# Kernel tuning notes

Hardware: AMD Instinct MI355X
Metric: run time of the kernel (lower is better)

## Reference

```python
import jax, jax.numpy as jnp
import numpy as np

B, N, C_FEAT = 2, 1024, 64
S, K, K_FP = 512, 32, 3
D_MODEL, N_HEAD = 128, 4
EPS_BN = 1e-5


def square_distance(src, dst):
    # src [B,N,3], dst [B,M,3] -> [B,N,M], same expansion as torch version
    d = -2.0 * jnp.einsum('bnc,bmc->bnm', src, dst)
    d = d + jnp.sum(src ** 2, -1)[:, :, None]
    d = d + jnp.sum(dst ** 2, -1)[:, None, :]
    return d


def gather_points(points, idx):
    # points [B,N,C], idx [B,...] int -> [B,...,C]  (index_points)
    return jax.vmap(lambda p, i: p[i])(points, idx)


def fps(xyz, n_samples):
    # furthest point sampling, deterministic start at index 0
    Bs, Np, _ = xyz.shape
    def step(carry, _):
        dist, far = carry
        centroid = jax.vmap(lambda p, i: p[i])(xyz, far)  # [B,3]
        d = jnp.sum((xyz - centroid[:, None, :]) ** 2, -1)
        dist = jnp.minimum(dist, d)
        new_far = jnp.argmax(dist, -1).astype(jnp.int32)
        return (dist, new_far), far
    init = (jnp.full((Bs, Np), 1e10, xyz.dtype), jnp.zeros((Bs,), jnp.int32))
    _, idxs = jax.lax.scan(step, init, None, length=n_samples)
    return idxs.T  # [B,S]


def knn(nsample, xyz, new_xyz):
    d = square_distance(new_xyz, xyz)
    _, idx = jax.lax.top_k(-d, nsample)
    return idx  # [B, n_query, nsample]


def setup_inputs() -> dict:
    key = jax.random.key(0)
    ks = jax.random.split(key, 12)
    Din = 2 * C_FEAT + 3  # 131 = 3 + 2*channels (PreExtraction in_channels)
    def lin(k, fan_in, shape):
        return (jax.random.normal(k, shape, jnp.float32) / np.sqrt(fan_in)).astype(jnp.float32)
    z = lambda n: jnp.zeros((n,), jnp.float32)
    return {
        'xyz': jax.random.normal(ks[0], (B, N, 3), jnp.float32),
        'feats': jax.random.normal(ks[1], (B, N, C_FEAT), jnp.float32),
        'affine_alpha': jnp.ones((1, 1, 1, C_FEAT + 3), jnp.float32),
        'affine_beta': jnp.zeros((1, 1, 1, C_FEAT + 3), jnp.float32),
        'W_t': lin(ks[2], Din, (Din, D_MODEL)), 'b_t': z(D_MODEL),
        'bn_g': jnp.ones((D_MODEL,), jnp.float32), 'bn_b': z(D_MODEL),
        'Wq': lin(ks[3], D_MODEL, (D_MODEL, D_MODEL)), 'bq': z(D_MODEL),
        'Wk': lin(ks[4], D_MODEL, (D_MODEL, D_MODEL)), 'bk': z(D_MODEL),
        'Wv': lin(ks[5], D_MODEL, (D_MODEL, D_MODEL)), 'bv': z(D_MODEL),
        'Wo': lin(ks[6], D_MODEL, (D_MODEL, D_MODEL)), 'bo': z(D_MODEL),
        'Wp1': lin(ks[7], 3, (3, D_MODEL)), 'bp1': z(D_MODEL),
        'Wp2': lin(ks[8], D_MODEL, (D_MODEL, N_HEAD)), 'bp2': z(N_HEAD),
    }


def reference(xyz, feats, affine_alpha, affine_beta, W_t, b_t, bn_g, bn_b,
              Wq, bq, Wk, bk, Wv, bv, Wo, bo, Wp1, bp1, Wp2, bp2):
    # ---- LocalGrouper (FPS + KNN + gather + center-normalize + affine) ----
    fps_idx = fps(xyz, S)                       # [B,S]
    new_xyz = gather_points(xyz, fps_idx)       # [B,S,3]
    anchor_feats = gather_points(feats, fps_idx)  # [B,S,C]
    idx = knn(K, xyz, new_xyz)                  # [B,S,K]
    grouped_xyz = gather_points(xyz, idx)       # [B,S,K,3]
    grouped_pts = gather_points(feats, idx)     # [B,S,K,C]
    grouped = jnp.concatenate([grouped_pts, grouped_xyz], -1)  # [B,S,K,C+3]
    mean = jnp.mean(grouped, axis=2, keepdims=True)
    std = jnp.std((grouped - mean).reshape(B, -1), axis=-1, ddof=1)[:, None, None, None]
    grouped = (grouped - mean) / (std + 1e-5)
    grouped = affine_alpha * grouped + affine_beta
    anchor_rep = jnp.broadcast_to(anchor_feats[:, :, None, :], (B, S, K, C_FEAT))
    new_points = jnp.concatenate([grouped, anchor_rep], -1)  # [B,S,K,2C+3]
    # ---- PreExtraction transfer (1x1 conv + BN(eval) + ReLU) + max over K ----
    y = jnp.einsum('bskd,do->bsko', new_points, W_t) + b_t
    y = y * (bn_g / jnp.sqrt(1.0 + EPS_BN)) + bn_b  # BN with running stats (0,1)
    y = jax.nn.relu(y)
    v_k = jnp.max(y, axis=2)                    # [B,S,D_MODEL]
    # ---- PointNetFeaturePropagation (KNN-3 inverse-distance interp) ----
    idx_fp = knn(K_FP, new_xyz, xyz)            # [B,N,3]
    sqrd = square_distance(xyz, new_xyz)        # [B,N,S]
    d_near = jnp.clip(jnp.take_along_axis(sqrd, idx_fp, axis=2), 1e-10, None)
    w = 1.0 / d_near
    w = w / jnp.sum(w, -1, keepdims=True)
    grouped_v = gather_points(v_k, idx_fp)      # [B,N,3,D]
    v_q = jnp.einsum('bnk,bnkc->bnc', w, grouped_v)  # [B,N,D]
    # ---- PointTransformerCrossAttention ----
    Dh = D_MODEL // N_HEAD
    qh = (v_q @ Wq + bq).reshape(B, N, N_HEAD, Dh)
    kh = (v_k @ Wk + bk).reshape(B, S, N_HEAD, Dh)
    vh = (v_k @ Wv + bv).reshape(B, S, N_HEAD, Dh)
    rel = xyz[:, :, None, :] - new_xyz[:, None, :, :]         # [B,N,S,3]
    rpe = jax.nn.relu(rel @ Wp1 + bp1) @ Wp2 + bp2            # [B,N,S,H]
    energy = jnp.einsum('bihd,bjhd->bhij', qh, kh) / jnp.sqrt(jnp.float32(Dh))
    attn = jax.nn.softmax(energy + rpe.transpose(0, 3, 1, 2), axis=-1)
    out = jnp.einsum('bhij,bjhd->bihd', attn, vh).reshape(B, N, D_MODEL)
    return out @ Wo + bo
```

## Files before the change

### kernel.cpp

```cpp
#include <hip/hip_runtime.h>
#include <math.h>

namespace {

constexpr int B  = 2;
constexpr int N  = 1024;
constexpr int CF = 64;
constexpr int S  = 512;
constexpr int K  = 32;
constexpr int DM = 128;
constexpr int NH = 4;
constexpr int DH = 32;
constexpr int GC = 67;
constexpr int DIN = 131;
constexpr int DPAD = 132;
constexpr int EPAD = 516;

typedef float f2 __attribute__((ext_vector_type(2)));

__device__ inline float max3f(float a, float b, float c) { return fmaxf(fmaxf(a, b), c); }
__device__ inline unsigned min3u(unsigned a, unsigned b, unsigned c) { return min(min(a, b), c); }

template <int CTRL>
__device__ inline float dpp_mov_f(float v) {
  return __int_as_float(__builtin_amdgcn_update_dpp(0, __float_as_int(v), CTRL, 0xF, 0xF, true));
}
template <int CTRL>
__device__ inline unsigned dpp_mov_self_u(unsigned v) {
  return (unsigned)__builtin_amdgcn_update_dpp((int)v, (int)v, CTRL, 0xF, 0xF, false);
}

__global__ void __launch_bounds__(64, 1)
fps_kernel(const float* __restrict__ xyz, int* __restrict__ fps_idx,
           float* __restrict__ new_xyz) {
  const int b = blockIdx.x;
  const int lane = threadIdx.x;
  __shared__ __align__(16) float4 pts4[N];
  __shared__ int farhist[S];
  for (int p = lane; p < N; p += 64) {
    pts4[p] = make_float4(xyz[b*N*3 + p*3+0], xyz[b*N*3 + p*3+1], xyz[b*N*3 + p*3+2], 0.0f);
  }
  __syncthreads();
  f2 X[8], Y[8], Z[8];
  float dist[16];
  #pragma unroll
  for (int j = 0; j < 8; ++j) {
    const float4 a = pts4[(2*j)*64 + lane];
    const float4 c = pts4[(2*j+1)*64 + lane];
    X[j] = f2{a.x, c.x}; Y[j] = f2{a.y, c.y}; Z[j] = f2{a.z, c.z};
  }
  #pragma unroll
  for (int k = 0; k < 16; ++k) dist[k] = 1e10f;
  int far = 0;
  for (int s = 0; s < S; ++s) {
    if (lane == 0) farhist[s] = far;
    const float4 c = pts4[far];
    const f2 cx = f2{c.x, c.x}, cy = f2{c.y, c.y}, cz = f2{c.z, c.z};
    #pragma unroll
    for (int j = 0; j < 8; ++j) {
      const f2 dx = X[j] - cx, dy = Y[j] - cy, dz = Z[j] - cz;
      const f2 q = dx*dx + dy*dy + dz*dz;
      dist[2*j]   = fminf(dist[2*j],   q.x);
      dist[2*j+1] = fminf(dist[2*j+1], q.y);
    }
    const float l0 = max3f(dist[0],  dist[1],  dist[2]);
    const float l1 = max3f(dist[3],  dist[4],  dist[5]);
    const float l2 = max3f(dist[6],  dist[7],  dist[8]);
    const float l3 = max3f(dist[9],  dist[10], dist[11]);
    const float l4 = max3f(dist[12], dist[13], dist[14]);
    float mv = fmaxf(max3f(l0, l1, l2), max3f(l3, l4, dist[15]));
    mv = fmaxf(mv, dpp_mov_f<0x111>(mv));
    mv = fmaxf(mv, dpp_mov_f<0x112>(mv));
    mv = fmaxf(mv, dpp_mov_f<0x114>(mv));
    mv = fmaxf(mv, dpp_mov_f<0x118>(mv));
    mv = fmaxf(mv, dpp_mov_f<0x142>(mv));
    mv = fmaxf(mv, dpp_mov_f<0x143>(mv));
    const float maxv = __int_as_float(__builtin_amdgcn_readlane(__float_as_int(mv), 63));
    unsigned cnd[16];
    #pragma unroll
    for (int k = 0; k < 16; ++k) {
      cnd[k] = (dist[k] == maxv) ? (unsigned)(k*64 + lane) : 0xFFFFFFFFu;
    }
    const unsigned u0 = min3u(cnd[0],  cnd[1],  cnd[2]);
    const unsigned u1 = min3u(cnd[3],  cnd[4],  cnd[5]);
    const unsigned u2 = min3u(cnd[6],  cnd[7],  cnd[8]);
    const unsigned u3 = min3u(cnd[9],  cnd[10], cnd[11]);
    const unsigned u4 = min3u(cnd[12], cnd[13], cnd[14]);
    unsigned cand = min(min3u(u0, u1, u2), min3u(u3, u4, cnd[15]));
    cand = min(cand, dpp_mov_self_u<0x111>(cand));
    cand = min(cand, dpp_mov_self_u<0x112>(cand));
    cand = min(cand, dpp_mov_self_u<0x114>(cand));
    cand = min(cand, dpp_mov_self_u<0x118>(cand));
    cand = min(cand, dpp_mov_self_u<0x142>(cand));
    cand = min(cand, dpp_mov_self_u<0x143>(cand));
    far = __builtin_amdgcn_readlane((int)cand, 63);
  }
  __syncthreads();
  for (int s = lane; s < S; s += 64) {
    const int f = farhist[s];
    const float4 c = pts4[f];
    fps_idx[b*S+s] = f;
    new_xyz[(b*S+s)*3+0] = c.x;
    new_xyz[(b*S+s)*3+1] = c.y;
    new_xyz[(b*S+s)*3+2] = c.z;
  }
}

__global__ void knn_kernel(const float* __restrict__ xyz, const float* __restrict__ new_xyz,
                           int* __restrict__ knn_idx) {
  const int b = blockIdx.y;
  const int tid = threadIdx.x;
  const int wave = tid >> 6, lane = tid & 63;
  const int s = blockIdx.x * 4 + wave;
  __shared__ float pts[N*3];
  for (int i = tid; i < N*3; i += 256) pts[i] = xyz[b*N*3 + i];
  __syncthreads();
  const float qx = new_xyz[(b*S+s)*3+0], qy = new_xyz[(b*S+s)*3+1], qz = new_xyz[(b*S+s)*3+2];
  const float qn = qx*qx + qy*qy + qz*qz;
  float d[16];
  #pragma unroll
  for (int j = 0; j < 16; ++j) {
    const int p = j*64 + lane;
    const float px = pts[p*3+0], py = pts[p*3+1], pz = pts[p*3+2];
    const float dot = qx*px + qy*py + qz*pz;
    const float pn  = px*px + py*py + pz*pz;
    d[j] = (-2.0f*dot + qn) + pn;
  }
  unsigned mask = 0xFFFFu;
  for (int k = 0; k < K; ++k) {
    float bv = INFINITY; int bj = 0;
    #pragma unroll
    for (int j = 0; j < 16; ++j) {
      if (((mask >> j) & 1u) && d[j] < bv) { bv = d[j]; bj = j; }
    }
    int bp = bj*64 + lane;
    #pragma unroll
    for (int m = 1; m < 64; m <<= 1) {
      const float ov = __shfl_xor(bv, m);
      const int   op = __shfl_xor(bp, m);
      if (ov < bv || (ov == bv && op < bp)) { bv = ov; bp = op; }
    }
    if (lane == 0) knn_idx[(b*S+s)*K + k] = bp;
    if ((bp & 63) == lane) mask &= ~(1u << (bp >> 6));
  }
}

__global__ void group_stats_kernel(const float* __restrict__ feats, const float* __restrict__ xyz,
                                   const int* __restrict__ knn_idx, float* __restrict__ mean_out,
                                   float2* __restrict__ partials) {
  const int bs = blockIdx.x;
  const int b = bs / S;
  const int t = threadIdx.x;
  __shared__ int sidx[K];
  if (t < K) sidx[t] = knn_idx[bs*K + t];
  __syncthreads();
  float v[K];
  float ls = 0.0f, lsq = 0.0f;
  if (t < GC) {
    float sum = 0.0f;
    #pragma unroll
    for (int k = 0; k < K; ++k) {
      const int p = sidx[k];
      const float g = (t < CF) ? feats[(b*N+p)*CF + t] : xyz[(b*N+p)*3 + (t-CF)];
      v[k] = g; sum += g;
    }
    const float mean = sum * (1.0f/K);
    mean_out[bs*GC + t] = mean;
    #pragma unroll
    for (int k = 0; k < K; ++k) {
      const float c = v[k] - mean;
      ls += c; lsq += c*c;
    }
  }
  __shared__ float r1[128], r2[128];
  r1[t] = ls; r2[t] = lsq;
  __syncthreads();
  for (int off = 64; off >= 1; off >>= 1) {
    if (t < off) { r1[t] += r1[t+off]; r2[t] += r2[t+off]; }
    __syncthreads();
  }
  if (t == 0) partials[bs] = make_float2(r1[0], r2[0]);
}

__global__ void stats_kernel(const float2* __restrict__ partials, float* __restrict__ invstd) {
  const int b = blockIdx.x;
  const int lane = threadIdx.x;
  double su = 0.0, sq = 0.0;
  for (int i = lane; i < S; i += 64) {
    const float2 p = partials[b*S+i];
    su += (double)p.x; sq += (double)p.y;
  }
  #pragma unroll
  for (int m = 1; m < 64; m <<= 1) { su += __shfl_xor(su, m); sq += __shfl_xor(sq, m); }
  if (lane == 0) {
    const double nn = (double)S * K * GC;
    const double var = (sq - su*su/nn) / (nn - 1.0);
    invstd[b] = 1.0f / ((float)sqrt(var) + 1e-5f);
  }
}

__global__ void transfer_kernel(const float* __restrict__ feats, const float* __restrict__ xyz,
                                const int* __restrict__ knn_idx, const int* __restrict__ fps_idx,
                                const float* __restrict__ mean_in, const float* __restrict__ invstd,
                                const float* __restrict__ alpha, const float* __restrict__ beta,
                                const float* __restrict__ W_t, const float* __restrict__ b_t,
                                const float* __restrict__ bn_g, const float* __restrict__ bn_b,
                                const float* __restrict__ Wk, const float* __restrict__ bk,
                                const float* __restrict__ Wv, const float* __restrict__ bv,
                                float* __restrict__ v_k, float* __restrict__ kpb,
                                float* __restrict__ vpb) {
  const int bs = blockIdx.x;
  const int b = bs / S;
  const int t = threadIdx.x;
  __shared__ __align__(16) float np_s[K][DPAD];
  __shared__ float vrow[DM];
  __shared__ int sidx[K];
  __shared__ int sanchor;
  if (t < K) sidx[t] = knn_idx[bs*K + t];
  if (t == 0) sanchor = fps_idx[bs];
  __syncthreads();
  const float sinv = invstd[b];
  for (int k = 0; k < K; ++k) {
    const int p = sidx[k];
    for (int c = t; c < DPAD; c += 128) {
      float val = 0.0f;
      if (c < GC) {
        const float g = (c < CF) ? feats[(b*N+p)*CF + c] : xyz[(b*N+p)*3 + (c-CF)];
        val = (g - mean_in[bs*GC + c]) * sinv * alpha[c] + beta[c];
      } else if (c < DIN) {
        val = feats[(b*N+sanchor)*CF + (c - GC)];
      }
      np_s[k][c] = val;
    }
  }
  __syncthreads();
  float acc[K];
  const float bt = b_t[t];
  #pragma unroll
  for (int k = 0; k < K; ++k) acc[k] = bt;
  for (int d4 = 0; d4 < DPAD/4; ++d4) {
    const int d = d4*4;
    const float w0 = W_t[(d+0)*DM + t];
    const float w1 = W_t[(d+1)*DM + t];
    const float w2 = W_t[(d+2)*DM + t];
    const float w3 = (d+3 < DIN) ? W_t[(d+3)*DM + t] : 0.0f;
    #pragma unroll
    for (int k = 0; k < K; ++k) {
      const float4 f = *reinterpret_cast<const float4*>(&np_s[k][d]);
      acc[k] = acc[k] + f.x*w0 + f.y*w1 + f.z*w2 + f.w*w3;
    }
  }
  const float scale = bn_g[t] / sqrtf(1.0f + 1e-5f);
  const float shift = bn_b[t];
  float mx = -INFINITY;
  #pragma unroll
  for (int k = 0; k < K; ++k) {
    const float y = fmaxf(acc[k]*scale + shift, 0.0f);
    mx = fmaxf(mx, y);
  }
  v_k[bs*DM + t] = mx;
  vrow[t] = mx;
  __syncthreads();
  float acck = bk[t], accv = bv[t];
  for (int d = 0; d < DM; ++d) {
    const float f = vrow[d];
    acck += f * Wk[d*DM + t];
    accv += f * Wv[d*DM + t];
  }
  kpb[bs*DM + t] = acck;
  vpb[bs*DM + t] = accv;
}

__global__ void interp_kernel(const float* __restrict__ xyz, const float* __restrict__ new_xyz,
                              const float* __restrict__ v_k, const float* __restrict__ Wq,
                              const float* __restrict__ bq, float* __restrict__ qbuf) {
  const int b = blockIdx.y;
  const int tid = threadIdx.x;
  const int wave = tid >> 6, lane = tid & 63;
  const int n = blockIdx.x*4 + wave;
  __shared__ float pts[S*3];
  __shared__ float vqs[4][DM];
  for (int i = tid; i < S*3; i += 256) pts[i] = xyz ? new_xyz[b*S*3 + i] : 0.0f;
  __syncthreads();
  const float qx = xyz[(b*N+n)*3+0], qy = xyz[(b*N+n)*3+1], qz = xyz[(b*N+n)*3+2];
  const float qn = qx*qx + qy*qy + qz*qz;
  float d[8];
  #pragma unroll
  for (int j = 0; j < 8; ++j) {
    const int p = j*64 + lane;
    const float px = pts[p*3+0], py = pts[p*3+1], pz = pts[p*3+2];
    const float dot = qx*px + qy*py + qz*pz;
    const float pn  = px*px + py*py + pz*pz;
    d[j] = (-2.0f*dot + qn) + pn;
  }
  unsigned mask = 0xFFu;
  float sd[3]; int sp[3];
  #pragma unroll
  for (int k = 0; k < 3; ++k) {
    float bv = INFINITY; int bj = 0;
    #pragma unroll
    for (int j = 0; j < 8; ++j) {
      if (((mask >> j) & 1u) && d[j] < bv) { bv = d[j]; bj = j; }
    }
    int bp = bj*64 + lane;
    #pragma unroll
    for (int m = 1; m < 64; m <<= 1) {
      const float ov = __shfl_xor(bv, m);
      const int   op = __shfl_xor(bp, m);
      if (ov < bv || (ov == bv && op < bp)) { bv = ov; bp = op; }
    }
    sd[k] = bv; sp[k] = bp;
    if ((bp & 63) == lane) mask &= ~(1u << (bp >> 6));
  }
  float w0 = 1.0f / fmaxf(sd[0], 1e-10f);
  float w1 = 1.0f / fmaxf(sd[1], 1e-10f);
  float w2 = 1.0f / fmaxf(sd[2], 1e-10f);
  const float wsum = w0 + w1 + w2;
  w0 /= wsum; w1 /= wsum; w2 /= wsum;
  const float* vk0 = v_k + (b*S + sp[0])*DM;
  const float* vk1 = v_k + (b*S + sp[1])*DM;
  const float* vk2 = v_k + (b*S + sp[2])*DM;
  #pragma unroll
  for (int c = lane; c < DM; c += 64) {
    vqs[wave][c] = w0*vk0[c] + w1*vk1[c] + w2*vk2[c];
  }
  __syncthreads();
  const float* row = vqs[wave];
  #pragma unroll
  for (int half = 0; half < 2; ++half) {
    const int c = lane + half*64;
    float acc = bq[c];
    for (int d = 0; d < DM; ++d) acc += row[d] * Wq[d*DM + c];
    qbuf[(b*N+n)*DM + c] = acc;
  }
}

__global__ void attn_kernel(const float* __restrict__ xyz, const float* __restrict__ new_xyz,
                            const float* __restrict__ qb, const float* __restrict__ kp,
                            const float* __restrict__ vp, const float* __restrict__ Wp1,
                            const float* __restrict__ bp1, const float* __restrict__ Wp2,
                            const float* __restrict__ bp2, const float* __restrict__ Wo,
                            const float* __restrict__ bo, float* __restrict__ out) {
  const int bn = blockIdx.x;
  const int b = bn / N;
  const int t = threadIdx.x;
  __shared__ __align__(16) float e[NH][EPAD];
  __shared__ float qn_s[DM];
  __shared__ float oa[DM];
  __shared__ float ssum[NH];
  qn_s[t] = qb[bn*DM + t];
  __syncthreads();
  const float qx = xyz[bn*3+0], qy = xyz[bn*3+1], qz = xyz[bn*3+2];
  const float rs = 0.17677669529663687f;
  for (int j = t; j < S; j += 128) {
    const float px = new_xyz[(b*S+j)*3+0], py = new_xyz[(b*S+j)*3+1], pz = new_xyz[(b*S+j)*3+2];
    const float rx = qx-px, ry = qy-py, rz = qz-pz;
    float r0 = bp2[0], r1 = bp2[1], r2 = bp2[2], r3 = bp2[3];
    for (int m = 0; m < DM; ++m) {
      float hm = rx*Wp1[m] + ry*Wp1[DM+m] + rz*Wp1[2*DM+m] + bp1[m];
      hm = fmaxf(hm, 0.0f);
      r0 += hm*Wp2[m*NH+0]; r1 += hm*Wp2[m*NH+1];
      r2 += hm*Wp2[m*NH+2]; r3 += hm*Wp2[m*NH+3];
    }
    const float rpe[NH] = {r0, r1, r2, r3};
    #pragma unroll
    for (int h = 0; h < NH; ++h) {
      const float* kr = kp + (b*S+j)*DM + h*DH;
      const float* qr = qn_s + h*DH;
      float acc = 0.0f;
      #pragma unroll
      for (int dd = 0; dd < DH; ++dd) acc += qr[dd]*kr[dd];
      e[h][j] = acc*rs + rpe[h];
    }
  }
  __syncthreads();
  const int h = t >> 5, g = t & 31;
  float mx = -INFINITY;
  for (int j = g; j < S; j += 32) mx = fmaxf(mx, e[h][j]);
  #pragma unroll
  for (int m = 16; m >= 1; m >>= 1) mx = fmaxf(mx, __shfl_xor(mx, m));
  float sum = 0.0f;
  for (int j = g; j < S; j += 32) { const float ex = expf(e[h][j]-mx); e[h][j] = ex; sum += ex; }
  #pragma unroll
  for (int m = 16; m >= 1; m >>= 1) sum += __shfl_xor(sum, m);
  if (g == 0) ssum[h] = sum;
  __syncthreads();
  float acc = 0.0f;
  for (int j = 0; j < S; j += 4) {
    const float4 ev = *reinterpret_cast<const float4*>(&e[h][j]);
    acc += ev.x * vp[(b*S+j+0)*DM + t];
    acc += ev.y * vp[(b*S+j+1)*DM + t];
    acc += ev.z * vp[(b*S+j+2)*DM + t];
    acc += ev.w * vp[(b*S+j+3)*DM + t];
  }
  oa[t] = acc / ssum[h];
  __syncthreads();
  float facc = bo[t];
  for (int d = 0; d < DM; ++d) facc += oa[d] * Wo[d*DM + t];
  out[bn*DM + t] = facc;
}

}

extern "C" void kernel_launch(void* const* d_in, const int* in_sizes, int n_in,
                              void* d_out, int out_size, void* d_ws, size_t ws_size,
                              hipStream_t stream) {
  const float* xyz   = (const float*)d_in[0];
  const float* feats = (const float*)d_in[1];
  const float* alpha = (const float*)d_in[2];
  const float* beta  = (const float*)d_in[3];
  const float* W_t   = (const float*)d_in[4];
  const float* b_t   = (const float*)d_in[5];
  const float* bn_g  = (const float*)d_in[6];
  const float* bn_b  = (const float*)d_in[7];
  const float* Wq = (const float*)d_in[8];  const float* bq = (const float*)d_in[9];
  const float* Wk = (const float*)d_in[10]; const float* bk = (const float*)d_in[11];
  const float* Wv = (const float*)d_in[12]; const float* bv = (const float*)d_in[13];
  const float* Wo = (const float*)d_in[14]; const float* bo = (const float*)d_in[15];
  const float* Wp1= (const float*)d_in[16]; const float* bp1= (const float*)d_in[17];
  const float* Wp2= (const float*)d_in[18]; const float* bp2= (const float*)d_in[19];

  char* w = (char*)d_ws;
  int*    fps_i = (int*)   (w + 0);
  float*  nxyz  = (float*) (w + 4096);
  int*    knn_i = (int*)   (w + 16384);
  float*  meanb = (float*) (w + 147456);
  float2* part  = (float2*)(w + 421888);
  float*  invs  = (float*) (w + 430080);
  float*  vk    = (float*) (w + 430336);
  float*  qbuf  = (float*) (w + 2003200);
  float*  kpb   = (float*) (w + 3051776);
  float*  vpb   = (float*) (w + 3576064);
  float*  outf  = (float*)d_out;

  fps_kernel<<<B, 64, 0, stream>>>(xyz, fps_i, nxyz);
  knn_kernel<<<dim3(S/4, B), 256, 0, stream>>>(xyz, nxyz, knn_i);
  group_stats_kernel<<<B*S, 128, 0, stream>>>(feats, xyz, knn_i, meanb, part);
  stats_kernel<<<B, 64, 0, stream>>>(part, invs);
  transfer_kernel<<<B*S, 128, 0, stream>>>(feats, xyz, knn_i, fps_i, meanb, invs,
                                           alpha, beta, W_t, b_t, bn_g, bn_b,
                                           Wk, bk, Wv, bv, vk, kpb, vpb);
  interp_kernel<<<dim3(N/4, B), 256, 0, stream>>>(xyz, nxyz, vk, Wq, bq, qbuf);
  attn_kernel<<<B*N, 128, 0, stream>>>(xyz, nxyz, qbuf, kpb, vpb, Wp1, bp1, Wp2, bp2, Wo, bo, outf);
}
```

Measured before the change: 452.7 us.

## Fuse group stats into KNN kernel and merge FPS argmax reductions

FPS now does a single DPP reduction over a packed (distance bits, inverted index) pair instead of two sequential reductions (max value, then min index), which shortens the serial per-iteration critical path. The group-statistics kernel is folded into the KNN kernel: each wave uses its freshly selected neighbor indices from shared memory to compute per-channel means and centered sums, reduced with wave shuffles. This removes one launch and a global re-read of knn indices, at the cost of more work per KNN wave. The float-bit ordering relies on distances being non-negative.

```diff
diff --git a/kernel.cpp b/kernel.cpp
--- a/kernel.cpp
+++ b/kernel.cpp
@@ -22,12 +22,12 @@
 __device__ inline unsigned min3u(unsigned a, unsigned b, unsigned c) { return min(min(a, b), c); }
 
 template <int CTRL>
-__device__ inline float dpp_mov_f(float v) {
-  return __int_as_float(__builtin_amdgcn_update_dpp(0, __float_as_int(v), CTRL, 0xF, 0xF, true));
-}
-template <int CTRL>
-__device__ inline unsigned dpp_mov_self_u(unsigned v) {
-  return (unsigned)__builtin_amdgcn_update_dpp((int)v, (int)v, CTRL, 0xF, 0xF, false);
+__device__ inline void dpp_max64(unsigned &hi, unsigned &lo) {
+  const unsigned ohi = (unsigned)__builtin_amdgcn_update_dpp(0, (int)hi, CTRL, 0xF, 0xF, true);
+  const unsigned olo = (unsigned)__builtin_amdgcn_update_dpp(0, (int)lo, CTRL, 0xF, 0xF, true);
+  const bool gt = (ohi > hi) || ((ohi == hi) && (olo > lo));
+  hi = gt ? ohi : hi;
+  lo = gt ? olo : lo;
 }
 
 __global__ void __launch_bounds__(64, 1)
@@ -68,32 +68,27 @@
     const float l2 = max3f(dist[6],  dist[7],  dist[8]);
     const float l3 = max3f(dist[9],  dist[10], dist[11]);
     const float l4 = max3f(dist[12], dist[13], dist[14]);
-    float mv = fmaxf(max3f(l0, l1, l2), max3f(l3, l4, dist[15]));
-    mv = fmaxf(mv, dpp_mov_f<0x111>(mv));
-    mv = fmaxf(mv, dpp_mov_f<0x112>(mv));
-    mv = fmaxf(mv, dpp_mov_f<0x114>(mv));
-    mv = fmaxf(mv, dpp_mov_f<0x118>(mv));
-    mv = fmaxf(mv, dpp_mov_f<0x142>(mv));
-    mv = fmaxf(mv, dpp_mov_f<0x143>(mv));
-    const float maxv = __int_as_float(__builtin_amdgcn_readlane(__float_as_int(mv), 63));
+    const float mv = fmaxf(max3f(l0, l1, l2), max3f(l3, l4, dist[15]));
     unsigned cnd[16];
     #pragma unroll
     for (int k = 0; k < 16; ++k) {
-      cnd[k] = (dist[k] == maxv) ? (unsigned)(k*64 + lane) : 0xFFFFFFFFu;
+      cnd[k] = (dist[k] == mv) ? (unsigned)(k*64 + lane) : 0xFFFFFFFFu;
     }
     const unsigned u0 = min3u(cnd[0],  cnd[1],  cnd[2]);
     const unsigned u1 = min3u(cnd[3],  cnd[4],  cnd[5]);
     const unsigned u2 = min3u(cnd[6],  cnd[7],  cnd[8]);
     const unsigned u3 = min3u(cnd[9],  cnd[10], cnd[11]);
     const unsigned u4 = min3u(cnd[12], cnd[13], cnd[14]);
-    unsigned cand = min(min3u(u0, u1, u2), min3u(u3, u4, cnd[15]));
-    cand = min(cand, dpp_mov_self_u<0x111>(cand));
-    cand = min(cand, dpp_mov_self_u<0x112>(cand));
-    cand = min(cand, dpp_mov_self_u<0x114>(cand));
-    cand = min(cand, dpp_mov_self_u<0x118>(cand));
-    cand = min(cand, dpp_mov_self_u<0x142>(cand));
-    cand = min(cand, dpp_mov_self_u<0x143>(cand));
-    far = __builtin_amdgcn_readlane((int)cand, 63);
+    const unsigned locidx = min(min3u(u0, u1, u2), min3u(u3, u4, cnd[15]));
+    unsigned hi = __float_as_uint(mv);
+    unsigned lo = ~locidx;
+    dpp_max64<0x111>(hi, lo);
+    dpp_max64<0x112>(hi, lo);
+    dpp_max64<0x114>(hi, lo);
+    dpp_max64<0x118>(hi, lo);
+    dpp_max64<0x142>(hi, lo);
+    dpp_max64<0x143>(hi, lo);
+    far = (int)~(unsigned)__builtin_amdgcn_readlane((int)lo, 63);
   }
   __syncthreads();
   for (int s = lane; s < S; s += 64) {
@@ -106,13 +101,15 @@
   }
 }
 
-__global__ void knn_kernel(const float* __restrict__ xyz, const float* __restrict__ new_xyz,
-                           int* __restrict__ knn_idx) {
+__global__ void knn_kernel(const float* __restrict__ xyz, const float* __restrict__ feats,
+                           const float* __restrict__ new_xyz, int* __restrict__ knn_idx,
+                           float* __restrict__ mean_out, float2* __restrict__ partials) {
   const int b = blockIdx.y;
   const int tid = threadIdx.x;
   const int wave = tid >> 6, lane = tid & 63;
   const int s = blockIdx.x * 4 + wave;
   __shared__ float pts[N*3];
+  __shared__ int sidx_s[4][K];
   for (int i = tid; i < N*3; i += 256) pts[i] = xyz[b*N*3 + i];
   __syncthreads();
   const float qx = new_xyz[(b*S+s)*3+0], qy = new_xyz[(b*S+s)*3+1], qz = new_xyz[(b*S+s)*3+2];
@@ -140,46 +137,49 @@
       const int   op = __shfl_xor(bp, m);
       if (ov < bv || (ov == bv && op < bp)) { bv = ov; bp = op; }
     }
-    if (lane == 0) knn_idx[(b*S+s)*K + k] = bp;
+    if (lane == 0) { knn_idx[(b*S+s)*K + k] = bp; sidx_s[wave][k] = bp; }
     if ((bp & 63) == lane) mask &= ~(1u << (bp >> 6));
   }
-}
-
-__global__ void group_stats_kernel(const float* __restrict__ feats, const float* __restrict__ xyz,
-                                   const int* __restrict__ knn_idx, float* __restrict__ mean_out,
-                                   float2* __restrict__ partials) {
-  const int bs = blockIdx.x;
-  const int b = bs / S;
-  const int t = threadIdx.x;
-  __shared__ int sidx[K];
-  if (t < K) sidx[t] = knn_idx[bs*K + t];
-  __syncthreads();
+  const int bs = b*S + s;
+  float ls = 0.0f, lsq = 0.0f;
   float v[K];
-  float ls = 0.0f, lsq = 0.0f;
-  if (t < GC) {
+  {
+    const int c = lane;
     float sum = 0.0f;
     #pragma unroll
     for (int k = 0; k < K; ++k) {
-      const int p = sidx[k];
-      const float g = (t < CF) ? feats[(b*N+p)*CF + t] : xyz[(b*N+p)*3 + (t-CF)];
+      const int p = sidx_s[wave][k];
+      const float g = feats[(b*N+p)*CF + c];
       v[k] = g; sum += g;
     }
     const float mean = sum * (1.0f/K);
-    mean_out[bs*GC + t] = mean;
+    mean_out[bs*GC + c] = mean;
     #pragma unroll
     for (int k = 0; k < K; ++k) {
-      const float c = v[k] - mean;
-      ls += c; lsq += c*c;
-    }
-  }
-  __shared__ float r1[128], r2[128];
-  r1[t] = ls; r2[t] = lsq;
-  __syncthreads();
-  for (int off = 64; off >= 1; off >>= 1) {
-    if (t < off) { r1[t] += r1[t+off]; r2[t] += r2[t+off]; }
-    __syncthreads();
-  }
-  if (t == 0) partials[bs] = make_float2(r1[0], r2[0]);
+      const float cc = v[k] - mean;
+      ls += cc; lsq += cc*cc;
+    }
+  }
+  if (lane < 3) {
+    const int c = CF + lane;
+    float sum = 0.0f;
+    #pragma unroll
+    for (int k = 0; k < K; ++k) {
+      const int p = sidx_s[wave][k];
+      const float g = xyz[(b*N+p)*3 + lane];
+      v[k] = g; sum += g;
+    }
+    const float mean = sum * (1.0f/K);
+    mean_out[bs*GC + c] = mean;
+    #pragma unroll
+    for (int k = 0; k < K; ++k) {
+      const float cc = v[k] - mean;
+      ls += cc; lsq += cc*cc;
+    }
+  }
+  #pragma unroll
+  for (int m = 1; m < 64; m <<= 1) { ls += __shfl_xor(ls, m); lsq += __shfl_xor(lsq, m); }
+  if (lane == 0) partials[bs] = make_float2(ls, lsq);
 }
 
 __global__ void stats_kernel(const float2* __restrict__ partials, float* __restrict__ invstd) {
@@ -280,7 +280,7 @@
   const int n = blockIdx.x*4 + wave;
   __shared__ float pts[S*3];
   __shared__ float vqs[4][DM];
-  for (int i = tid; i < S*3; i += 256) pts[i] = xyz ? new_xyz[b*S*3 + i] : 0.0f;
+  for (int i = tid; i < S*3; i += 256) pts[i] = new_xyz[b*S*3 + i];
   __syncthreads();
   const float qx = xyz[(b*N+n)*3+0], qy = xyz[(b*N+n)*3+1], qz = xyz[(b*N+n)*3+2];
   const float qn = qx*qx + qy*qy + qz*qz;
@@ -434,8 +434,7 @@
   float*  outf  = (float*)d_out;
 
   fps_kernel<<<B, 64, 0, stream>>>(xyz, fps_i, nxyz);
-  knn_kernel<<<dim3(S/4, B), 256, 0, stream>>>(xyz, nxyz, knn_i);
-  group_stats_kernel<<<B*S, 128, 0, stream>>>(feats, xyz, knn_i, meanb, part);
+  knn_kernel<<<dim3(S/4, B), 256, 0, stream>>>(xyz, feats, nxyz, knn_i, meanb, part);
   stats_kernel<<<B, 64, 0, stream>>>(part, invs);
   transfer_kernel<<<B*S, 128, 0, stream>>>(feats, xyz, knn_i, fps_i, meanb, invs,
                                            alpha, beta, W_t, b_t, bn_g, bn_b,
```

Result: slower. 477.5 us (+5.5%).
